# Kernel optimization log

Measured on AMD Instinct MI355X. Metric: run time of the kernel, lower is better.

Reference implementation:

```python
import jax, jax.numpy as jnp
import numpy as np

KS = 3      # kernel_size
PAD = 1     # padding
STRIDE = 1  # stride


def conv2d(x, w, b, stride, pad):
    out = jax.lax.conv_general_dilated(
        x, w, (stride, stride), [(pad, pad), (pad, pad)],
        dimension_numbers=("NCHW", "OIHW", "NCHW"))
    return out + b[None, :, None, None]


def setup_inputs() -> dict:
    key = jax.random.key(0)
    k1, k2, k3, k4, k5 = jax.random.split(key, 5)
    B, C, H, W, OUTC = 4, 64, 128, 128, 64
    x = jax.random.normal(k1, (B, C, H, W), jnp.float32)
    # offset-predicting conv (2*ks*ks output channels, 3x3, pad 1). Small scale
    # so sampled offsets stay in a realistic sub-pixel range.
    p_w = jax.random.normal(k2, (2 * KS * KS, C, 3, 3), jnp.float32) * 0.01
    p_b = jax.random.normal(k3, (2 * KS * KS,), jnp.float32) * 0.01
    # final conv: kernel ks, stride ks over the ks-expanded sampled map
    conv_w = jax.random.normal(k4, (OUTC, C, KS, KS), jnp.float32) * (1.0 / np.sqrt(C * KS * KS))
    conv_b = jax.random.normal(k5, (OUTC,), jnp.float32) * 0.01
    return {"x": x, "p_w": p_w, "p_b": p_b, "conv_w": conv_w, "conv_b": conv_b}


def deform_forward(x, p_w, p_b, conv_w, conv_b):
    ks = KS
    N = ks * ks
    offset = conv2d(x, p_w, p_b, STRIDE, 1)          # [B, 2N, h, w]
    B, _, h, w = offset.shape
    xp = jnp.pad(x, ((0, 0), (0, 0), (PAD, PAD), (PAD, PAD)))
    C, Hp, Wp = xp.shape[1], xp.shape[2], xp.shape[3]

    # sampling locations p = p_0 + p_n + offset   (channels-last: [B,h,w,N])
    r = jnp.arange(-(ks - 1) // 2, (ks - 1) // 2 + 1, dtype=jnp.float32)
    pnx = jnp.repeat(r, ks)[None, None, None, :]     # kernel row offsets (row-major)
    pny = jnp.tile(r, ks)[None, None, None, :]       # kernel col offsets
    p0x = jnp.arange(1, h * STRIDE + 1, STRIDE, dtype=jnp.float32)[None, :, None, None]
    p0y = jnp.arange(1, w * STRIDE + 1, STRIDE, dtype=jnp.float32)[None, None, :, None]
    off = jnp.transpose(offset, (0, 2, 3, 1))        # [B,h,w,2N]
    px = off[..., :N] + p0x + pnx                    # [B,h,w,N]
    py = off[..., N:] + p0y + pny

    # integer corner coords (detached in the torch original)
    fx = jnp.floor(jax.lax.stop_gradient(px))
    fy = jnp.floor(jax.lax.stop_gradient(py))
    qltx = jnp.clip(fx, 0, Hp - 1).astype(jnp.int32)
    qrbx = jnp.clip(fx + 1, 0, Hp - 1).astype(jnp.int32)
    qlty = jnp.clip(fy, 0, Wp - 1).astype(jnp.int32)
    qrby = jnp.clip(fy + 1, 0, Wp - 1).astype(jnp.int32)

    pxc = jnp.clip(px, 0, Hp - 1)
    pyc = jnp.clip(py, 0, Wp - 1)

    # bilinear weights (same signs/ordering as the torch code)
    glt = (1 + (qltx - pxc)) * (1 + (qlty - pyc))
    grb = (1 - (qrbx - pxc)) * (1 - (qrby - pyc))
    glb = (1 + (qltx - pxc)) * (1 - (qrby - pyc))
    grt = (1 - (qrbx - pxc)) * (1 + (qlty - pyc))

    bidx = jnp.arange(B).reshape(B, 1, 1, 1)

    def gat(qx, qy):
        # xp[b, :, qx, qy] -> [B,h,w,N,C] -> [B,C,h,w,N]
        g = xp[bidx, :, qx, qy]
        return jnp.moveaxis(g, -1, 1)

    x_off = (glt[:, None] * gat(qltx, qlty)
             + grb[:, None] * gat(qrbx, qrby)
             + glb[:, None] * gat(qltx, qrby)
             + grt[:, None] * gat(qrbx, qlty))        # [B,C,h,w,N]

    # rearrange 'b c h w (kx ky) -> b c (h kx) (w ky)'
    x_off = x_off.reshape(B, C, h, w, ks, ks).transpose(0, 1, 2, 4, 3, 5)
    x_off = x_off.reshape(B, C, h * ks, w * ks)
    return conv2d(x_off, conv_w, conv_b, ks, 0)      # [B,outc,h,w]


def reference(x, p_w, p_b, conv_w, conv_b):
    return deform_forward(x, p_w, p_b, conv_w, conv_b)
```

## Files before the change

kernel.cpp:

```cpp
#include <hip/hip_runtime.h>
#include <math.h>

#define CWTF_OFF 8388608
#define PWTF_OFF (CWTF_OFF + 73728)

typedef __attribute__((ext_vector_type(8))) _Float16 half8;
typedef __attribute__((ext_vector_type(8))) unsigned short ushort8;
typedef __attribute__((ext_vector_type(4))) float f32x4;
typedef __attribute__((ext_vector_type(4))) unsigned int u32x4;

__device__ inline unsigned short f2h(float f) {
    _Float16 h = (_Float16)f; return __builtin_bit_cast(unsigned short, h);
}

__global__ __launch_bounds__(256) void k_prep(const float* __restrict__ x,
                                              unsigned int* __restrict__ x_t_u32,
                                              const float* __restrict__ conv_w,
                                              const float* __restrict__ p_w,
                                              unsigned short* __restrict__ cwtf,
                                              unsigned short* __restrict__ pwtf) {
    if (blockIdx.x < 512) {
        __shared__ float t[64][129];
        int b = blockIdx.x >> 7;
        int i = blockIdx.x & 127;
        for (int idx = threadIdx.x; idx < 64 * 128; idx += 256) {
            int c = idx >> 7, j = idx & 127;
            t[c][j] = x[(((size_t)(b * 64 + c) * 128 + i) << 7) + j];
        }
        __syncthreads();
        unsigned int* dst = x_t_u32 + ((size_t)(b * 128 + i)) * 128 * 32;
        for (int idx2 = threadIdx.x; idx2 < 4096; idx2 += 256) {
            int j = idx2 >> 5, c2 = idx2 & 31;
            unsigned int lo = f2h(t[2 * c2][j]);
            unsigned int hi = f2h(t[2 * c2 + 1][j]);
            dst[idx2] = lo | (hi << 16);
        }
    } else {
        int tid = (blockIdx.x - 512) * 256 + threadIdx.x;
        if (tid < 36864) {
            int e = tid & 7, lane = (tid >> 3) & 63, nb = (tid >> 9) & 3, h = (tid >> 11) & 1, n = tid >> 12;
            int o = nb * 16 + (lane & 15);
            int c = h * 32 + ((lane >> 4) << 3) + e;
            cwtf[tid] = f2h(conv_w[(o * 64 + c) * 9 + n]);
        } else if (tid < 36864 + 18432) {
            int t2 = tid - 36864;
            int e = t2 & 7, lane = (t2 >> 3) & 63, nb = (t2 >> 9) & 1, h = (t2 >> 10) & 1, n = t2 >> 11;
            int np = nb * 16 + (lane & 15);
            int c = h * 32 + ((lane >> 4) << 3) + e;
            pwtf[t2] = (np < 18) ? f2h(p_w[(np * 64 + c) * 9 + n]) : (unsigned short)0;
        }
    }
}

#define TROWS 7
#define TCOLS 71
#define TRECS (TROWS * TCOLS)
#define TILE_B (TRECS * 128)
#define OFF_OFFS TILE_B
#define OFF_GEOM (TILE_B + 4608)
#define OFF_FLAG (TILE_B + 4608 + 9216)

__global__ __launch_bounds__(512, 2) void k_fused(const unsigned short* __restrict__ x_t,
                                                  const unsigned short* __restrict__ cwtf,
                                                  const unsigned short* __restrict__ pwtf,
                                                  const float* __restrict__ p_b,
                                                  const float* __restrict__ conv_b,
                                                  float* __restrict__ out) {
    __shared__ __align__(16) unsigned char S[TILE_B + 4608 + 9216 + 16];
    unsigned char* tile = S;
    float* offs = (float*)(S + OFF_OFFS);
    unsigned char* geomB = S + OFF_GEOM;
    int* flagp = (int*)(S + OFF_FLAG);

    int bid0 = blockIdx.x;
    int bid = (bid0 & 7) * 128 + (bid0 >> 3);
    int b = bid >> 8;
    int i = (bid >> 1) & 127;
    int j0 = (bid & 1) << 6;
    int ib = i - 3, jb = j0 - 3;

    int tid = threadIdx.x;
    int lane = tid & 63;
    int r15 = lane & 15;
    int g = lane >> 4;
    int wv = tid >> 6;
    int pg = wv & 3;
    int h = wv >> 2;
    int pl = pg * 16 + r15;
    int cs = g + (h << 2);
    int csx = cs << 4;

    if (tid == 0) *flagp = 0;

    for (int u = tid; u < TRECS * 8; u += 512) {
        int rec = u >> 3, chunk = u & 7;
        int trow = rec / TCOLS;
        int tcol = rec - trow * TCOLS;
        int gr = ib + trow, gc = jb + tcol;
        bool v = ((unsigned)gr < 128u) && ((unsigned)gc < 128u);
        int grc = v ? gr : 0, gcc = v ? gc : 0;
        ushort8 val = *(const ushort8*)(x_t + (((size_t)((b * 128 + grc) * 128 + gcc)) << 6) + (chunk << 3));
        if (!v) val = (ushort8)(unsigned short)0;
        *(ushort8*)(tile + rec * 128 + ((chunk ^ (rec & 7)) << 4)) = val;
    }
    __syncthreads();

    f32x4 aco0 = (f32x4)0.f, aco1 = (f32x4)0.f;
    for (int n = 0; n < 9; ++n) {
        int du = n / 3 - 1, dv = n % 3 - 1;
        int trec = (du + 3) * TCOLS + (pl + dv + 3);
        int xb = trec & 7;
        half8 a = *(const half8*)(tile + trec * 128 + ((cs ^ xb) << 4));
        const unsigned short* pb = pwtf + (((n * 2 + h) * 2) << 9) + (lane << 3);
        half8 b0 = *(const half8*)pb;
        half8 b1 = *(const half8*)(pb + 512);
        aco0 = __builtin_amdgcn_mfma_f32_16x16x32_f16(a, b0, aco0, 0, 0, 0);
        aco1 = __builtin_amdgcn_mfma_f32_16x16x32_f16(a, b1, aco1, 0, 0, 0);
    }
#pragma unroll
    for (int hh = 0; hh < 2; ++hh) {
        if (h == hh) {
#pragma unroll
            for (int nb = 0; nb < 2; ++nb) {
                int np = nb * 16 + r15;
                if (np < 18) {
                    f32x4 a = nb ? aco1 : aco0;
#pragma unroll
                    for (int rr = 0; rr < 4; ++rr) {
                        int pix = pg * 16 + g * 4 + rr;
                        if (hh == 0)
                            offs[pix * 18 + np] = a[rr] + p_b[np];
                        else
                            offs[pix * 18 + np] += a[rr];
                    }
                }
            }
        }
        __syncthreads();
    }

    for (int t = tid; t < 576; t += 512) {
        int p = t / 9;
        int n = t - p * 9;
        float ox = offs[p * 18 + n];
        float oy = offs[p * 18 + 9 + n];
        float px = ox + (float)(i + 1) + (float)(n / 3 - 1);
        float py = oy + (float)(j0 + p + 1) + (float)(n % 3 - 1);
        float fx = floorf(px), fy = floorf(py);
        float qlx = fminf(fmaxf(fx, 0.f), 129.f);
        float qrx = fminf(fmaxf(fx + 1.f, 0.f), 129.f);
        float qly = fminf(fmaxf(fy, 0.f), 129.f);
        float qry = fminf(fmaxf(fy + 1.f, 0.f), 129.f);
        float pxc = fminf(fmaxf(px, 0.f), 129.f);
        float pyc = fminf(fmaxf(py, 0.f), 129.f);
        float ax = 1.f + qlx - pxc;
        float bx = 1.f - qrx + pxc;
        float ay = 1.f + qly - pyc;
        float by = 1.f - qry + pyc;
        int rlx = (int)qlx - 1, rrx = (int)qrx - 1;
        int rly = (int)qly - 1, rry = (int)qry - 1;
        bool bad = false;
        unsigned int pk[4];
        int cx[4] = {rlx, rrx, rlx, rrx};
        int cy[4] = {rly, rry, rry, rly};
        float cw[4] = {ax * ay, bx * by, ax * by, bx * ay};
#pragma unroll
        for (int k = 0; k < 4; ++k) {
            bool v = ((unsigned)cx[k] < 128u) && ((unsigned)cy[k] < 128u);
            bool intile = (((unsigned)(cx[k] - ib) < (unsigned)TROWS) &&
                           ((unsigned)(cy[k] - jb) < (unsigned)TCOLS));
            unsigned rec = (unsigned)(cx[k] - ib) * TCOLS + (unsigned)(cy[k] - jb);
            pk[k] = (v && intile) ? (((rec * 8u + (rec & 7u)) << 16) | f2h(cw[k])) : 0u;
            bad = bad || (v && !intile);
        }
        *(u32x4*)(geomB + ((n * 64 + p) << 4)) = (u32x4){pk[0], pk[1], pk[2], pk[3]};
        if (bad) *flagp = 1;
    }
    __syncthreads();

    f32x4 acc[4];
#pragma unroll
    for (int nb = 0; nb < 4; ++nb) acc[nb] = (f32x4)0.f;
    bool fast = (*flagp == 0);

    if (fast) {
        for (int n = 0; n < 9; ++n) {
            u32x4 gq = *(const u32x4*)(geomB + ((n * 64 + pl) << 4));
            half8 Bf[4];
#pragma unroll
            for (int nb = 0; nb < 4; ++nb)
                Bf[nb] = *(const half8*)(cwtf + ((((n * 2 + h) << 2) + nb) << 9) + (lane << 3));
            half8 av = (half8)(_Float16)0;
#pragma unroll
            for (int k = 0; k < 4; ++k) {
                unsigned int p = gq[k];
                _Float16 wk = __builtin_bit_cast(_Float16, (unsigned short)(p & 0xFFFFu));
                half8 u = *(const half8*)(tile + (((p >> 16) << 4) ^ (unsigned)csx));
                av += u * wk;
            }
#pragma unroll
            for (int nb = 0; nb < 4; ++nb)
                acc[nb] = __builtin_amdgcn_mfma_f32_16x16x32_f16(av, Bf[nb], acc[nb], 0, 0, 0);
        }
    } else {
        for (int n = 0; n < 9; ++n) {
            half8 Bf[4];
#pragma unroll
            for (int nb = 0; nb < 4; ++nb)
                Bf[nb] = *(const half8*)(cwtf + ((((n * 2 + h) << 2) + nb) << 9) + (lane << 3));
            float ox = offs[pl * 18 + n];
            float oy = offs[pl * 18 + 9 + n];
            float px = ox + (float)(i + 1) + (float)(n / 3 - 1);
            float py = oy + (float)(j0 + pl + 1) + (float)(n % 3 - 1);
            float fx = floorf(px), fy = floorf(py);
            float qlx = fminf(fmaxf(fx, 0.f), 129.f);
            float qrx = fminf(fmaxf(fx + 1.f, 0.f), 129.f);
            float qly = fminf(fmaxf(fy, 0.f), 129.f);
            float qry = fminf(fmaxf(fy + 1.f, 0.f), 129.f);
            float pxc = fminf(fmaxf(px, 0.f), 129.f);
            float pyc = fminf(fmaxf(py, 0.f), 129.f);
            float ax = 1.f + qlx - pxc;
            float bx = 1.f - qrx + pxc;
            float ay = 1.f + qly - pyc;
            float by = 1.f - qry + pyc;
            int cx[4] = {(int)qlx - 1, (int)qrx - 1, (int)qlx - 1, (int)qrx - 1};
            int cy[4] = {(int)qly - 1, (int)qry - 1, (int)qry - 1, (int)qly - 1};
            float cw[4] = {ax * ay, bx * by, ax * by, bx * ay};
            half8 av = (half8)(_Float16)0;
#pragma unroll
            for (int k = 0; k < 4; ++k) {
                bool v = ((unsigned)cx[k] < 128u) && ((unsigned)cy[k] < 128u);
                size_t base = v ? (((size_t)((b * 128 + cx[k]) * 128 + cy[k])) << 6) : 0;
                _Float16 wk = v ? (_Float16)cw[k] : (_Float16)0.f;
                half8 u = *(const half8*)(x_t + base + (cs << 3));
                av += u * wk;
            }
#pragma unroll
            for (int nb = 0; nb < 4; ++nb)
                acc[nb] = __builtin_amdgcn_mfma_f32_16x16x32_f16(av, Bf[nb], acc[nb], 0, 0, 0);
        }
    }
    __syncthreads();

    {
        float* epH = (float*)(S + (h ? 16640 : 0));
#pragma unroll
        for (int nb = 0; nb < 4; ++nb) {
            int o = nb * 16 + r15;
#pragma unroll
            for (int rr = 0; rr < 4; ++rr) {
                int pix = pg * 16 + g * 4 + rr;
                epH[o * 65 + pix] = acc[nb][rr];
            }
        }
    }
    __syncthreads();
    {
        float* e0 = (float*)S;
        float* e1 = (float*)(S + 16640);
        for (int t = tid; t < 4096; t += 512) {
            int o = t >> 6;
            int p = t & 63;
            out[(((size_t)(b * 64 + o)) << 14) + (i << 7) + j0 + p] =
                e0[o * 65 + p] + e1[o * 65 + p] + conv_b[o];
        }
    }
}

extern "C" void kernel_launch(void* const* d_in, const int* in_sizes, int n_in,
                              void* d_out, int out_size, void* d_ws, size_t ws_size,
                              hipStream_t stream) {
    const float* x = (const float*)d_in[0];
    const float* p_w = (const float*)d_in[1];
    const float* p_b = (const float*)d_in[2];
    const float* conv_w = (const float*)d_in[3];
    const float* conv_b = (const float*)d_in[4];
    float* out = (float*)d_out;
    char* ws = (char*)d_ws;

    unsigned short* x_t = (unsigned short*)(ws);
    unsigned short* cwtf = (unsigned short*)(ws + CWTF_OFF);
    unsigned short* pwtf = (unsigned short*)(ws + PWTF_OFF);

    k_prep<<<728, 256, 0, stream>>>(x, (unsigned int*)x_t, conv_w, p_w, cwtf, pwtf);
    k_fused<<<1024, 512, 0, stream>>>(x_t, cwtf, pwtf, p_b, conv_b, out);
}
```

Measured before the change: 38.47 us.

## Switch main conv MFMA from 16x16x32 to 32x32x16 tiles with K-split waves

Reorganizes the final-conv matrix multiply to use 32x32x16 f16 MFMA instructions: each wave now covers 32 pixels by 64 output channels for a 16-channel K slice, instead of 16 pixels by 64 outputs for a 32-channel slice. The weight pre-transform layout is changed to match. Each wave now gathers and blends one sampled half8 per tap and issues two larger MFMAs instead of four small ones, which cuts weight-fragment loads and instruction count per tap. The cost is a four-way K split that needs a two-round shared-memory reduction in the epilogue, adding an extra barrier and read-modify-write traffic.

```diff
diff --git a/kernel.cpp b/kernel.cpp
--- a/kernel.cpp
+++ b/kernel.cpp
@@ -7,6 +7,7 @@
 typedef __attribute__((ext_vector_type(8))) _Float16 half8;
 typedef __attribute__((ext_vector_type(8))) unsigned short ushort8;
 typedef __attribute__((ext_vector_type(4))) float f32x4;
+typedef __attribute__((ext_vector_type(16))) float f32x16;
 typedef __attribute__((ext_vector_type(4))) unsigned int u32x4;
 
 __device__ inline unsigned short f2h(float f) {
@@ -38,9 +39,9 @@
     } else {
         int tid = (blockIdx.x - 512) * 256 + threadIdx.x;
         if (tid < 36864) {
-            int e = tid & 7, lane = (tid >> 3) & 63, nb = (tid >> 9) & 3, h = (tid >> 11) & 1, n = tid >> 12;
-            int o = nb * 16 + (lane & 15);
-            int c = h * 32 + ((lane >> 4) << 3) + e;
+            int e = tid & 7, lane = (tid >> 3) & 63, oh = (tid >> 9) & 1, kq = (tid >> 10) & 3, n = tid >> 12;
+            int o = oh * 32 + (lane & 31);
+            int c = kq * 16 + ((lane >> 5) << 3) + e;
             cwtf[tid] = f2h(conv_w[(o * 64 + c) * 9 + n]);
         } else if (tid < 36864 + 18432) {
             int t2 = tid - 36864;
@@ -88,7 +89,6 @@
     int h = wv >> 2;
     int pl = pg * 16 + r15;
     int cs = g + (h << 2);
-    int csx = cs << 4;
 
     if (tid == 0) *flagp = 0;
 
@@ -178,40 +178,40 @@
     }
     __syncthreads();
 
-    f32x4 acc[4];
-#pragma unroll
-    for (int nb = 0; nb < 4; ++nb) acc[nb] = (f32x4)0.f;
+    int pg2 = wv & 1;
+    int kq = wv >> 1;
+    int pl3 = pg2 * 32 + (lane & 31);
+    unsigned csx3 = (unsigned)((kq * 2 + (lane >> 5)) << 4);
+    f32x16 acc0 = (f32x16)0.f, acc1 = (f32x16)0.f;
     bool fast = (*flagp == 0);
 
     if (fast) {
         for (int n = 0; n < 9; ++n) {
-            u32x4 gq = *(const u32x4*)(geomB + ((n * 64 + pl) << 4));
-            half8 Bf[4];
-#pragma unroll
-            for (int nb = 0; nb < 4; ++nb)
-                Bf[nb] = *(const half8*)(cwtf + ((((n * 2 + h) << 2) + nb) << 9) + (lane << 3));
+            u32x4 gq = *(const u32x4*)(geomB + ((n * 64 + pl3) << 4));
+            const unsigned short* cb = cwtf + (((n * 4 + kq) * 2) << 9) + (lane << 3);
+            half8 Bf0 = *(const half8*)cb;
+            half8 Bf1 = *(const half8*)(cb + 512);
             half8 av = (half8)(_Float16)0;
 #pragma unroll
             for (int k = 0; k < 4; ++k) {
                 unsigned int p = gq[k];
                 _Float16 wk = __builtin_bit_cast(_Float16, (unsigned short)(p & 0xFFFFu));
-                half8 u = *(const half8*)(tile + (((p >> 16) << 4) ^ (unsigned)csx));
+                half8 u = *(const half8*)(tile + (((p >> 16) << 4) ^ csx3));
                 av += u * wk;
             }
-#pragma unroll
-            for (int nb = 0; nb < 4; ++nb)
-                acc[nb] = __builtin_amdgcn_mfma_f32_16x16x32_f16(av, Bf[nb], acc[nb], 0, 0, 0);
+            acc0 = __builtin_amdgcn_mfma_f32_32x32x16_f16(av, Bf0, acc0, 0, 0, 0);
+            acc1 = __builtin_amdgcn_mfma_f32_32x32x16_f16(av, Bf1, acc1, 0, 0, 0);
         }
     } else {
+        int cs3e = (kq * 2 + (lane >> 5)) << 3;
         for (int n = 0; n < 9; ++n) {
-            half8 Bf[4];
-#pragma unroll
-            for (int nb = 0; nb < 4; ++nb)
-                Bf[nb] = *(const half8*)(cwtf + ((((n * 2 + h) << 2) + nb) << 9) + (lane << 3));
-            float ox = offs[pl * 18 + n];
-            float oy = offs[pl * 18 + 9 + n];
+            const unsigned short* cb = cwtf + (((n * 4 + kq) * 2) << 9) + (lane << 3);
+            half8 Bf0 = *(const half8*)cb;
+            half8 Bf1 = *(const half8*)(cb + 512);
+            float ox = offs[pl3 * 18 + n];
+            float oy = offs[pl3 * 18 + 9 + n];
             float px = ox + (float)(i + 1) + (float)(n / 3 - 1);
-            float py = oy + (float)(j0 + pl + 1) + (float)(n % 3 - 1);
+            float py = oy + (float)(j0 + pl3 + 1) + (float)(n % 3 - 1);
             float fx = floorf(px), fy = floorf(py);
             float qlx = fminf(fmaxf(fx, 0.f), 129.f);
             float qrx = fminf(fmaxf(fx + 1.f, 0.f), 129.f);
@@ -232,29 +232,37 @@
                 bool v = ((unsigned)cx[k] < 128u) && ((unsigned)cy[k] < 128u);
                 size_t base = v ? (((size_t)((b * 128 + cx[k]) * 128 + cy[k])) << 6) : 0;
                 _Float16 wk = v ? (_Float16)cw[k] : (_Float16)0.f;
-                half8 u = *(const half8*)(x_t + base + (cs << 3));
+                half8 u = *(const half8*)(x_t + base + cs3e);
                 av += u * wk;
             }
-#pragma unroll
-            for (int nb = 0; nb < 4; ++nb)
-                acc[nb] = __builtin_amdgcn_mfma_f32_16x16x32_f16(av, Bf[nb], acc[nb], 0, 0, 0);
+            acc0 = __builtin_amdgcn_mfma_f32_32x32x16_f16(av, Bf0, acc0, 0, 0, 0);
+            acc1 = __builtin_amdgcn_mfma_f32_32x32x16_f16(av, Bf1, acc1, 0, 0, 0);
         }
     }
     __syncthreads();
 
     {
-        float* epH = (float*)(S + (h ? 16640 : 0));
-#pragma unroll
-        for (int nb = 0; nb < 4; ++nb) {
-            int o = nb * 16 + r15;
-#pragma unroll
-            for (int rr = 0; rr < 4; ++rr) {
-                int pix = pg * 16 + g * 4 + rr;
-                epH[o * 65 + pix] = acc[nb][rr];
-            }
-        }
-    }
-    __syncthreads();
+        float* epH = (float*)(S + ((kq >> 1) ? 16640 : 0));
+#pragma unroll
+        for (int round = 0; round < 2; ++round) {
+            if ((kq & 1) == round) {
+#pragma unroll
+                for (int oh = 0; oh < 2; ++oh) {
+                    int o = oh * 32 + (lane & 31);
+                    f32x16 a = oh ? acc1 : acc0;
+#pragma unroll
+                    for (int reg = 0; reg < 16; ++reg) {
+                        int pix = pg2 * 32 + ((reg & 3) + 8 * (reg >> 2) + 4 * (lane >> 5));
+                        if (round == 0)
+                            epH[o * 65 + pix] = a[reg];
+                        else
+                            epH[o * 65 + pix] += a[reg];
+                    }
+                }
+            }
+            __syncthreads();
+        }
+    }
     {
         float* e0 = (float*)S;
         float* e1 = (float*)(S + 16640);
```

Measured after the change: 38.26 us. Within noise of the previous version (-0.5%).
